# Kernel tuning notes

Measured on AMD Instinct MI355X. Metric: run time of the kernel, lower is better.

Reference implementation:

```python
import jax, jax.numpy as jnp
import numpy as np

VOCAB = 50257
D = 256
BATCH = 8


def setup_inputs() -> dict:
    key = jax.random.key(0)
    k1, k2, k3, k4, k5 = jax.random.split(key, 5)
    initial_ids = jax.random.randint(k1, (BATCH, 1), 0, VOCAB, dtype=jnp.int32)
    state = jax.random.normal(k2, (BATCH, D), dtype=jnp.float32)
    emb = jax.random.normal(k3, (VOCAB, D), dtype=jnp.float32) * 0.02
    W = jax.random.normal(k4, (D, VOCAB), dtype=jnp.float32) * 0.02
    U = jax.random.normal(k5, (D, D), dtype=jnp.float32) * 0.02
    return {"initial_ids": initial_ids, "state": state, "emb": emb,
            "W": W, "U": U, "beam_size": 32, "max_decode_length": 16}


def _logits_fn(ids, state, emb, W, U):
    # Stand-in for the external logits_fn: simple tanh-RNN cell + vocab projection.
    # ids: [b, beam, L], state: [b, beam, d]
    last = ids[:, :, -1]                                       # [b, beam]
    x = jnp.tanh(jnp.einsum('bkd,de->bke', state, U) + emb[last])  # [b, beam, d]
    token_scores = jax.nn.log_softmax(jnp.einsum('bkd,dv->bkv', x, W), axis=-1)
    return token_scores, x


def reference(initial_ids, state, emb, W, U, beam_size, max_decode_length):
    b = initial_ids.shape[0]
    vocab = W.shape[1]
    ids = initial_ids[:, None, :]                # [b, 1, L0]  (beam0 = 1)
    cache = state[:, None, :]                    # [b, 1, d]
    scores = jnp.zeros((b, 1), dtype=jnp.float32)
    for i in range(max_decode_length):           # unrolled, as in the TF original
        beam0 = ids.shape[1]
        token_scores, cache = _logits_fn(ids, cache, emb, W, U)   # [b,beam0,V]
        k = min(beam_size, beam0 * vocab)
        all_scores = (scores[:, :, None] + token_scores).reshape(b, beam0 * vocab)
        top_scores, top_ixs = jax.lax.top_k(all_scores, k)        # sorted, [b,k]
        top_beams = top_ixs // vocab                              # [b,k]
        top_tokens = top_ixs % vocab                              # [b,k]
        ids = jnp.take_along_axis(ids, top_beams[:, :, None], axis=1)
        ids = jnp.concatenate([ids, top_tokens[:, :, None].astype(ids.dtype)], axis=-1)
        cache = jnp.take_along_axis(cache, top_beams[:, :, None], axis=1)
        scores = top_scores
    return ids, scores
```

## Files before the change

kernel.cpp:

```cpp
#include <hip/hip_runtime.h>
#include <math.h>

#define B 8
#define D 256
#define V 50257
#define VP 50304
#define BEAM 32
#define STEPS 16
#define MAXLEN 17
#define FNEG_INF (-3.4e38f)
#define NG 1571
#define NSG 50
#define NSEG 197
#define NLCAP 800
#define SLOTCAP 1600

static_assert((V + 255) / 256 == NSEG, "NSEG mismatch");

struct SchedT {
    int nl, nops, nlev, root, minLeaf;
    int lvlStart[36];
    int leafOff[NLCAP];
    int leafN[NLCAP];
    int sA[NLCAP];
    int sB[NLCAP];
    int sD[NLCAP];
};

constexpr SchedT build_sched() {
    SchedT s{};
    int sOff[64] = {}, sN[64] = {}, sPh[64] = {};
    int vSlot[64] = {}, vLev[64] = {};
    int oA[NLCAP] = {}, oB[NLCAP] = {}, oD[NLCAP] = {}, oL[NLCAP] = {};
    int sp = 0, vp = 0, nl = 0, nops = 0;
    s.minLeaf = 1 << 30;
    sOff[0] = 0; sN[0] = V; sPh[0] = 0; sp = 1;
    while (sp) {
        int i = sp - 1;
        int n = sN[i];
        if (n <= 128) {
            s.leafOff[nl] = sOff[i]; s.leafN[nl] = n;
            if (n < s.minLeaf) s.minLeaf = n;
            vSlot[vp] = nl; vLev[vp] = 0; ++vp; ++nl; --sp; continue;
        }
        int n2 = (n / 2) - ((n / 2) % 8);
        int ph = sPh[i];
        if (ph == 0)      { sPh[i] = 1; sOff[sp] = sOff[i];      sN[sp] = n2;     sPh[sp] = 0; ++sp; }
        else if (ph == 1) { sPh[i] = 2; sOff[sp] = sOff[i] + n2; sN[sp] = n - n2; sPh[sp] = 0; ++sp; }
        else {
            int bI = --vp; int aI = --vp;
            int lev = (vLev[aI] > vLev[bI] ? vLev[aI] : vLev[bI]) + 1;
            oA[nops] = vSlot[aI]; oB[nops] = vSlot[bI]; oD[nops] = NLCAP + nops; oL[nops] = lev;
            vSlot[vp] = NLCAP + nops; vLev[vp] = lev; ++vp; ++nops; --sp;
        }
    }
    s.nl = nl; s.nops = nops; s.root = vSlot[0];
    int maxl = 0;
    for (int k = 0; k < nops; ++k) if (oL[k] > maxl) maxl = oL[k];
    s.nlev = maxl;
    int cnt[36] = {};
    for (int k = 0; k < nops; ++k) cnt[oL[k]]++;
    int run = 0;
    s.lvlStart[0] = 0;
    for (int k = 1; k <= maxl; ++k) { s.lvlStart[k] = run; run += cnt[k]; cnt[k] = s.lvlStart[k]; }
    s.lvlStart[maxl + 1] = run;
    for (int k = 0; k < nops; ++k) { int p = cnt[oL[k]]++; s.sA[p] = oA[k]; s.sB[p] = oB[k]; s.sD[p] = oD[k]; }
    return s;
}

constexpr SchedT SCH = build_sched();
static_assert(SCH.nl <= NLCAP, "leaf overflow");
static_assert(SCH.nops <= NLCAP, "op overflow");
static_assert(SCH.nlev <= 34, "level overflow");
static_assert(SCH.root < SLOTCAP, "slot overflow");
static_assert(SCH.minLeaf >= 8, "leaf < 8 would break 8-lane cluster sum");

__global__ void k_init(const int* __restrict__ initial_ids, const float* __restrict__ state,
                       float* __restrict__ cache, int* __restrict__ ids, float* __restrict__ scores) {
    int b = blockIdx.x, t = threadIdx.x;
    cache[b * D + t] = state[b * D + t];
    if (t == 0) { ids[b * MAXLEN] = initial_ids[b]; scores[b] = 0.f; }
}

__global__ __launch_bounds__(256) void k_embed(const float* __restrict__ cache, const int* __restrict__ ids,
                                               const float* __restrict__ emb, const float* __restrict__ U,
                                               float* __restrict__ x, int step) {
    int rr = blockIdx.x, j = threadIdx.x;
    __shared__ float sc[D];
    sc[j] = cache[rr * D + j];
    __syncthreads();
    int last = ids[rr * MAXLEN + step];
    float acc = 0.f;
    for (int d = 0; d < D; ++d)
        acc = __fadd_rn(acc, __fmul_rn(sc[d], U[d * D + j]));
    float pre = __fadd_rn(acc, emb[(size_t)last * D + j]);
    x[rr * D + j] = (float)tanh((double)pre);
}

__global__ __launch_bounds__(256) void k_trans(const float* __restrict__ x, float* __restrict__ xT) {
    __shared__ float tile[32][33];
    int t = threadIdx.x;
    int tx = t & 31, ty = t >> 5;
    int bx = blockIdx.x * 32, by = blockIdx.y * 32;
#pragma unroll
    for (int i = 0; i < 4; ++i)
        tile[ty + i * 8][tx] = x[(size_t)(by + ty + i * 8) * D + bx + tx];
    __syncthreads();
#pragma unroll
    for (int i = 0; i < 4; ++i)
        xT[(size_t)(bx + ty + i * 8) * 256 + by + tx] = tile[tx][ty + i * 8];
}

__global__ __launch_bounds__(256) void k_gemm(const float* __restrict__ xT, const float* __restrict__ W,
                                              float* __restrict__ L, float* __restrict__ segMax, int rows) {
    int t = threadIdx.x;
    int v = blockIdx.x * 256 + t;
    int r0 = blockIdx.y * 32;
    bool vok = (v < V);
    float acc[32];
#pragma unroll
    for (int r = 0; r < 32; ++r) acc[r] = 0.f;
    for (int d = 0; d < D; ++d) {
        float w = vok ? W[(size_t)d * V + v] : 0.f;
        const float* xp = xT + d * 256 + r0;
#pragma unroll
        for (int r = 0; r < 32; ++r)
            acc[r] = __fadd_rn(acc[r], __fmul_rn(xp[r], w));
    }
#pragma unroll
    for (int r = 0; r < 32; ++r)
        if (vok && r0 + r < rows) L[(size_t)(r0 + r) * VP + v] = acc[r];

    __shared__ float wmax[4][32];
    int wave = t >> 6, lane = t & 63;
#pragma unroll
    for (int r = 0; r < 32; ++r) {
        float mv = vok ? acc[r] : FNEG_INF;
#pragma unroll
        for (int o = 1; o < 64; o <<= 1) mv = fmaxf(mv, __shfl_xor(mv, o));
        if (lane == 0) wmax[wave][r] = mv;
    }
    __syncthreads();
    if (t < 32 && r0 + t < rows) {
        float mv = fmaxf(fmaxf(wmax[0][t], wmax[1][t]), fmaxf(wmax[2][t], wmax[3][t]));
        segMax[(size_t)(r0 + t) * NSEG + blockIdx.x] = mv;
    }
}

__device__ __forceinline__ float Ev(const float* __restrict__ a, float m, int i) {
    return (float)exp((double)__fsub_rn(a[i], m));
}

__global__ __launch_bounds__(1024) void k_post(const float* __restrict__ L, const float* __restrict__ segMax,
                                               const float* __restrict__ scores,
                                               float* __restrict__ candV, int* __restrict__ candI) {
    int rr = blockIdx.x, t = threadIdx.x;
    const float* Lr = L + (size_t)rr * VP;
    __shared__ float mS;
    __shared__ float vals[SLOTCAP];
    __shared__ float gval[NG]; __shared__ int gidx[NG]; __shared__ unsigned gmask[NG];
    __shared__ float gv2[NG]; __shared__ int gi2[NG];
    __shared__ float sgval[64]; __shared__ int sgtok[64]; __shared__ int sggrp[64];

    if (t < 64) {
        float mv = FNEG_INF;
        for (int s = t; s < NSEG; s += 64) mv = fmaxf(mv, segMax[(size_t)rr * NSEG + s]);
#pragma unroll
        for (int o = 1; o < 64; o <<= 1) mv = fmaxf(mv, __shfl_xor(mv, o));
        if (t == 0) mS = mv;
    }
    __syncthreads();
    float m = mS;

    int cl = t >> 3, j = t & 7;
    for (int l = cl; l < SCH.nl; l += 128) {
        int off = SCH.leafOff[l], n = SCH.leafN[l];
        int n8 = n - (n % 8);
        float r = Ev(Lr, m, off + j);
        for (int i = 8; i < n8; i += 8) r = __fadd_rn(r, Ev(Lr, m, off + i + j));
        float s1 = __fadd_rn(r,  __shfl_xor(r, 1));
        float s2 = __fadd_rn(s1, __shfl_xor(s1, 2));
        float s3 = __fadd_rn(s2, __shfl_xor(s2, 4));
        if (j == 0) {
            float res = s3;
            for (int i = n8; i < n; ++i) res = __fadd_rn(res, Ev(Lr, m, off + i));
            vals[l] = res;
        }
    }
    __syncthreads();
    for (int lev = 1; lev <= SCH.nlev; ++lev) {
        for (int i = SCH.lvlStart[lev] + t; i < SCH.lvlStart[lev + 1]; i += 1024)
            vals[SCH.sD[i]] = __fadd_rn(vals[SCH.sA[i]], vals[SCH.sB[i]]);
        __syncthreads();
    }
    float lsf = (float)log((double)vals[SCH.root]);
    float sc = scores[rr];

    int wv = t >> 6, ln = t & 63;
    for (int g2 = wv * 2; g2 < NG; g2 += 32) {
        int g = g2 + (ln >> 5);
        int col = g2 * 32 + ln;
        bool liveg = (g < NG);
        bool live = liveg && (col < V);
        float oval = live ? __fadd_rn(sc, __fsub_rn(__fsub_rn(Lr[col], m), lsf)) : FNEG_INF;
        int oix = live ? col : 0x7fffffff;
        float val = oval; int ix = oix;
#pragma unroll
        for (int o = 1; o < 32; o <<= 1) {
            float v2 = __shfl_xor(val, o);
            int i2 = __shfl_xor(ix, o);
            if (v2 > val || (v2 == val && i2 < ix)) { val = v2; ix = i2; }
        }
        float val2 = (oix == ix) ? FNEG_INF : oval;
        int ix2 = (oix == ix) ? 0x7fffffff : oix;
#pragma unroll
        for (int o = 1; o < 32; o <<= 1) {
            float v2 = __shfl_xor(val2, o);
            int i2 = __shfl_xor(ix2, o);
            if (v2 > val2 || (v2 == val2 && i2 < ix2)) { val2 = v2; ix2 = i2; }
        }
        if (liveg && (ln & 31) == 0) {
            gval[g] = val; gidx[g] = ix; gv2[g] = val2; gi2[g] = ix2; gmask[g] = 0u;
        }
    }
    __syncthreads();

    for (int s2 = wv * 2; s2 < NSG; s2 += 32) {
        int s = s2 + (ln >> 5);
        int g = s2 * 32 + ln;
        bool lives = (s < NSG);
        bool live = lives && (g < NG);
        float val = live ? gval[g] : FNEG_INF;
        int tok = live ? gidx[g] : 0x7fffffff;
        int grp = live ? g : -1;
#pragma unroll
        for (int o = 1; o < 32; o <<= 1) {
            float v2 = __shfl_xor(val, o);
            int t2 = __shfl_xor(tok, o);
            int g3 = __shfl_xor(grp, o);
            if (v2 > val || (v2 == val && t2 < tok)) { val = v2; tok = t2; grp = g3; }
        }
        if (lives && (ln & 31) == 0) { sgval[s] = val; sgtok[s] = tok; sggrp[s] = grp; }
    }
    __syncthreads();
    if (t >= 64) return;

    for (int it = 0; it < 32; ++it) {
        float val = (t < NSG) ? sgval[t] : FNEG_INF;
        int tok = (t < NSG) ? sgtok[t] : 0x7fffffff;
        int grp = (t < NSG) ? sggrp[t] : -1;
#pragma unroll
        for (int o = 1; o < 64; o <<= 1) {
            float v2 = __shfl_xor(val, o);
            int t2 = __shfl_xor(tok, o);
            int g3 = __shfl_xor(grp, o);
            if (v2 > val || (v2 == val && t2 < tok)) { val = v2; tok = t2; grp = g3; }
        }
        int gw = grp, tw = tok;
        unsigned oldmask = gmask[gw];
        unsigned newmask = oldmask | (1u << (tw & 31));
        if (t == 0) {
            candV[rr * 32 + it] = val;
            candI[rr * 32 + it] = tw;
            gmask[gw] = newmask;
        }
        if (__popc(oldmask) == 0) {
            if (t == 0) { gval[gw] = gv2[gw]; gidx[gw] = gi2[gw]; }
        } else {
            int col = gw * 32 + (t & 31);
            bool live = (col < V) && !((newmask >> (t & 31)) & 1u);
            float nv = live ? __fadd_rn(sc, __fsub_rn(__fsub_rn(Lr[col], m), lsf)) : FNEG_INF;
            int nix = live ? col : 0x7fffffff;
#pragma unroll
            for (int o = 1; o < 32; o <<= 1) {
                float v2 = __shfl_xor(nv, o);
                int i2 = __shfl_xor(nix, o);
                if (v2 > nv || (v2 == nv && i2 < nix)) { nv = v2; nix = i2; }
            }
            if (t == 0) { gval[gw] = nv; gidx[gw] = nix; }
        }
        int s = gw >> 5;
        int gg = s * 32 + (t & 31);
        bool lv = (gg < NG);
        float sv = lv ? gval[gg] : FNEG_INF;
        int st = lv ? gidx[gg] : 0x7fffffff;
        int sg2 = lv ? gg : -1;
#pragma unroll
        for (int o = 1; o < 32; o <<= 1) {
            float v2 = __shfl_xor(sv, o);
            int t2 = __shfl_xor(st, o);
            int g3 = __shfl_xor(sg2, o);
            if (v2 > sv || (v2 == sv && t2 < st)) { sv = v2; st = t2; sg2 = g3; }
        }
        if (t == 0) { sgval[s] = sv; sgtok[s] = st; sggrp[s] = sg2; }
    }
}

__global__ __launch_bounds__(256) void k_merge(const float* __restrict__ candV, const int* __restrict__ candI,
                                               float* __restrict__ scoresNxt,
                                               const int* __restrict__ idsCur, int* __restrict__ idsNxt,
                                               const float* __restrict__ x, float* __restrict__ cacheNxt,
                                               int beam0, int step) {
    int b = blockIdx.x, t = threadIdx.x;
    int n = beam0 * BEAM;
    __shared__ float mval[BEAM * BEAM]; __shared__ int mbeam[BEAM * BEAM]; __shared__ int mtok[BEAM * BEAM];
    __shared__ float rv[256]; __shared__ int rk[256]; __shared__ int rs[256];
    __shared__ float wval[BEAM]; __shared__ int wbeam[BEAM]; __shared__ int wtok[BEAM];

    for (int i = t; i < n; i += 256) {
        int beam = i >> 5;
        int rr = b * beam0 + beam;
        mval[i] = candV[rr * BEAM + (i & 31)];
        mbeam[i] = beam;
        mtok[i] = candI[rr * BEAM + (i & 31)];
    }
    __syncthreads();

    for (int it = 0; it < BEAM; ++it) {
        float bv = FNEG_INF; int bk = 0x7fffffff; int bs = -1;
        for (int i = t; i < n; i += 256) {
            float v = mval[i];
            int gi = mbeam[i] * V + mtok[i];
            if (v > bv || (v == bv && gi < bk)) { bv = v; bk = gi; bs = i; }
        }
        rv[t] = bv; rk[t] = bk; rs[t] = bs; __syncthreads();
        for (int o = 128; o > 0; o >>= 1) {
            if (t < o) {
                if (rv[t + o] > rv[t] || (rv[t + o] == rv[t] && rk[t + o] < rk[t])) {
                    rv[t] = rv[t + o]; rk[t] = rk[t + o]; rs[t] = rs[t + o];
                }
            }
            __syncthreads();
        }
        if (t == 0) {
            int w = rs[0];
            wval[it] = rv[0]; wbeam[it] = mbeam[w]; wtok[it] = mtok[w];
            mval[w] = FNEG_INF;
        }
        __syncthreads();
    }

    if (t < BEAM) {
        scoresNxt[b * BEAM + t] = wval[t];
        int src = b * beam0 + wbeam[t];
        for (int u = 0; u <= step; ++u)
            idsNxt[(b * BEAM + t) * MAXLEN + u] = idsCur[src * MAXLEN + u];
        idsNxt[(b * BEAM + t) * MAXLEN + step + 1] = wtok[t];
    }
    __syncthreads();
    for (int j = 0; j < BEAM; ++j) {
        int src = b * beam0 + wbeam[j];
        cacheNxt[(size_t)(b * BEAM + j) * D + t] = x[(size_t)src * D + t];
    }
}

__global__ void k_out(const int* __restrict__ ids, const float* __restrict__ scores, float* __restrict__ out) {
    int t = blockIdx.x * 256 + threadIdx.x;
    const int NI = B * BEAM * MAXLEN;
    if (t < NI) out[t] = (float)ids[t];
    else if (t < NI + B * BEAM) out[t] = scores[t - NI];
}

extern "C" void kernel_launch(void* const* d_in, const int* in_sizes, int n_in,
                              void* d_out, int out_size, void* d_ws, size_t ws_size,
                              hipStream_t stream) {
    const int* initial_ids = (const int*)d_in[0];
    const float* state = (const float*)d_in[1];
    const float* emb = (const float*)d_in[2];
    const float* W = (const float*)d_in[3];
    const float* U = (const float*)d_in[4];

    char* ws = (char*)d_ws;
    size_t off = 0;
    float* L = (float*)(ws + off);       off += (size_t)256 * VP * 4;
    float* x = (float*)(ws + off);       off += 256 * D * 4;
    float* xT = (float*)(ws + off);      off += 256 * D * 4;
    float* cacheA = (float*)(ws + off);  off += 256 * D * 4;
    float* cacheB = (float*)(ws + off);  off += 256 * D * 4;
    float* scoresA = (float*)(ws + off); off += 256 * 4;
    float* scoresB = (float*)(ws + off); off += 256 * 4;
    int* idsA = (int*)(ws + off);        off += 256 * MAXLEN * 4;
    int* idsB = (int*)(ws + off);        off += 256 * MAXLEN * 4;
    float* candV = (float*)(ws + off);   off += 256 * 32 * 4;
    int* candI = (int*)(ws + off);       off += 256 * 32 * 4;
    float* segMax = (float*)(ws + off);  off += (size_t)256 * NSEG * 4;

    if (ws_size < off) return;

    k_init<<<B, 256, 0, stream>>>(initial_ids, state, cacheA, idsA, scoresA);

    float* cCur = cacheA; float* cNxt = cacheB;
    float* sCur = scoresA; float* sNxt = scoresB;
    int* iCur = idsA; int* iNxt = idsB;

    for (int step = 0; step < STEPS; ++step) {
        int beam0 = (step == 0) ? 1 : BEAM;
        int rows = B * beam0;

        k_embed<<<rows, 256, 0, stream>>>(cCur, iCur, emb, U, x, step);

        dim3 gt(8, 8);
        k_trans<<<gt, 256, 0, stream>>>(x, xT);

        dim3 g(NSEG, (rows + 31) / 32);
        k_gemm<<<g, 256, 0, stream>>>(xT, W, L, segMax, rows);

        k_post<<<rows, 1024, 0, stream>>>(L, segMax, sCur, candV, candI);
        k_merge<<<B, 256, 0, stream>>>(candV, candI, sNxt, iCur, iNxt, x, cNxt, beam0, step);

        float* tf; int* ti;
        tf = cCur; cCur = cNxt; cNxt = tf;
        tf = sCur; sCur = sNxt; sNxt = tf;
        ti = iCur; iCur = iNxt; iNxt = ti;
    }

    k_out<<<(B * BEAM * MAXLEN + B * BEAM + 255) / 256, 256, 0, stream>>>(iCur, sCur, (float*)d_out);
}
```

Measured before the change: 4.882 ms.

## Split post-processing into two-half logsumexp kernel and LDS-staged top-k kernel

The single per-row post kernel becomes two kernels. k_lsf builds its summation schedule for each half of the vocabulary and runs both halves as separate blocks, giving twice as many blocks for the double-precision exp reduction. The split point equals the original tree's root split, so the summation order stays the same. k_top then stages the logits in chunks through a 64KB shared buffer and computes each group's top-2 with a per-thread scan instead of wave shuffles. The cost is an extra launch, the logits being read twice, and heavy shared-memory use that limits occupancy.

```diff
diff --git a/kernel.cpp b/kernel.cpp
--- a/kernel.cpp
+++ b/kernel.cpp
@@ -14,6 +14,8 @@
 #define NSEG 197
 #define NLCAP 800
 #define SLOTCAP 1600
+#define NSPLIT 25128
+#define CHUNK 16384
 
 static_assert((V + 255) / 256 == NSEG, "NSEG mismatch");
 
@@ -27,14 +29,14 @@
     int sD[NLCAP];
 };
 
-constexpr SchedT build_sched() {
+constexpr SchedT build_sched(int off0, int n0) {
     SchedT s{};
     int sOff[64] = {}, sN[64] = {}, sPh[64] = {};
     int vSlot[64] = {}, vLev[64] = {};
     int oA[NLCAP] = {}, oB[NLCAP] = {}, oD[NLCAP] = {}, oL[NLCAP] = {};
     int sp = 0, vp = 0, nl = 0, nops = 0;
     s.minLeaf = 1 << 30;
-    sOff[0] = 0; sN[0] = V; sPh[0] = 0; sp = 1;
+    sOff[0] = off0; sN[0] = n0; sPh[0] = 0; sp = 1;
     while (sp) {
         int i = sp - 1;
         int n = sN[i];
@@ -68,12 +70,12 @@
     return s;
 }
 
-constexpr SchedT SCH = build_sched();
-static_assert(SCH.nl <= NLCAP, "leaf overflow");
-static_assert(SCH.nops <= NLCAP, "op overflow");
-static_assert(SCH.nlev <= 34, "level overflow");
-static_assert(SCH.root < SLOTCAP, "slot overflow");
-static_assert(SCH.minLeaf >= 8, "leaf < 8 would break 8-lane cluster sum");
+constexpr SchedT SCHL = build_sched(0, NSPLIT);
+constexpr SchedT SCHR = build_sched(NSPLIT, V - NSPLIT);
+static_assert(SCHL.nl <= NLCAP && SCHR.nl <= NLCAP, "leaf overflow");
+static_assert(SCHL.nops <= NLCAP && SCHR.nops <= NLCAP, "op overflow");
+static_assert(SCHL.nlev <= 34 && SCHR.nlev <= 34, "level overflow");
+static_assert(SCHL.minLeaf >= 8 && SCHR.minLeaf >= 8, "leaf < 8 breaks 8-lane cluster");
 
 __global__ void k_init(const int* __restrict__ initial_ids, const float* __restrict__ state,
                        float* __restrict__ cache, int* __restrict__ ids, float* __restrict__ scores) {
@@ -151,16 +153,12 @@
     return (float)exp((double)__fsub_rn(a[i], m));
 }
 
-__global__ __launch_bounds__(1024) void k_post(const float* __restrict__ L, const float* __restrict__ segMax,
-                                               const float* __restrict__ scores,
-                                               float* __restrict__ candV, int* __restrict__ candI) {
-    int rr = blockIdx.x, t = threadIdx.x;
+__global__ __launch_bounds__(1024) void k_lsf(const float* __restrict__ L, const float* __restrict__ segMax,
+                                              float* __restrict__ pSum) {
+    int rr = blockIdx.x, half = blockIdx.y, t = threadIdx.x;
     const float* Lr = L + (size_t)rr * VP;
     __shared__ float mS;
     __shared__ float vals[SLOTCAP];
-    __shared__ float gval[NG]; __shared__ int gidx[NG]; __shared__ unsigned gmask[NG];
-    __shared__ float gv2[NG]; __shared__ int gi2[NG];
-    __shared__ float sgval[64]; __shared__ int sgtok[64]; __shared__ int sggrp[64];
 
     if (t < 64) {
         float mv = FNEG_INF;
@@ -172,9 +170,19 @@
     __syncthreads();
     float m = mS;
 
+    const int* leafOff = half ? SCHR.leafOff : SCHL.leafOff;
+    const int* leafN   = half ? SCHR.leafN   : SCHL.leafN;
+    const int* sA      = half ? SCHR.sA      : SCHL.sA;
+    const int* sB      = half ? SCHR.sB      : SCHL.sB;
+    const int* sD      = half ? SCHR.sD      : SCHL.sD;
+    const int* lvlStart= half ? SCHR.lvlStart: SCHL.lvlStart;
+    int nl   = half ? SCHR.nl   : SCHL.nl;
+    int nlev = half ? SCHR.nlev : SCHL.nlev;
+    int root = half ? SCHR.root : SCHL.root;
+
     int cl = t >> 3, j = t & 7;
-    for (int l = cl; l < SCH.nl; l += 128) {
-        int off = SCH.leafOff[l], n = SCH.leafN[l];
+    for (int l = cl; l < nl; l += 128) {
+        int off = leafOff[l], n = leafN[l];
         int n8 = n - (n % 8);
         float r = Ev(Lr, m, off + j);
         for (int i = 8; i < n8; i += 8) r = __fadd_rn(r, Ev(Lr, m, off + i + j));
@@ -188,43 +196,67 @@
         }
     }
     __syncthreads();
-    for (int lev = 1; lev <= SCH.nlev; ++lev) {
-        for (int i = SCH.lvlStart[lev] + t; i < SCH.lvlStart[lev + 1]; i += 1024)
-            vals[SCH.sD[i]] = __fadd_rn(vals[SCH.sA[i]], vals[SCH.sB[i]]);
+    for (int lev = 1; lev <= nlev; ++lev) {
+        for (int i = lvlStart[lev] + t; i < lvlStart[lev + 1]; i += 1024)
+            vals[sD[i]] = __fadd_rn(vals[sA[i]], vals[sB[i]]);
         __syncthreads();
     }
-    float lsf = (float)log((double)vals[SCH.root]);
+    if (t == 0) pSum[rr * 2 + half] = vals[root];
+}
+
+__global__ __launch_bounds__(1024) void k_top(const float* __restrict__ L, const float* __restrict__ segMax,
+                                              const float* __restrict__ pSum, const float* __restrict__ scores,
+                                              float* __restrict__ candV, int* __restrict__ candI) {
+    int rr = blockIdx.x, t = threadIdx.x;
+    const float* Lr = L + (size_t)rr * VP;
+    __shared__ float mS;
+    __shared__ float buf[CHUNK];
+    __shared__ float gval[NG]; __shared__ int gidx[NG]; __shared__ unsigned gmask[NG];
+    __shared__ float gv2[NG]; __shared__ int gi2[NG];
+    __shared__ float sgval[64]; __shared__ int sgtok[64]; __shared__ int sggrp[64];
+
+    if (t < 64) {
+        float mv = FNEG_INF;
+        for (int s = t; s < NSEG; s += 64) mv = fmaxf(mv, segMax[(size_t)rr * NSEG + s]);
+#pragma unroll
+        for (int o = 1; o < 64; o <<= 1) mv = fmaxf(mv, __shfl_xor(mv, o));
+        if (t == 0) mS = mv;
+    }
+    __syncthreads();
+    float m = mS;
+    float lsf = (float)log((double)__fadd_rn(pSum[rr * 2 + 0], pSum[rr * 2 + 1]));
     float sc = scores[rr];
 
+    for (int c = 0; c < (V + CHUNK - 1) / CHUNK; ++c) {
+        int base = c * CHUNK;
+        int cnt = V - base; if (cnt > CHUNK) cnt = CHUNK;
+        int cnt4 = (cnt + 3) >> 2;
+        const float4* L4 = (const float4*)(Lr + base);
+        float4* B4 = (float4*)buf;
+        for (int i = t; i < cnt4; i += 1024) B4[i] = L4[i];
+        __syncthreads();
+        int gBase = base >> 5;
+        int gCnt = (cnt + 31) >> 5;
+        for (int g = gBase + t; g < gBase + gCnt; g += 1024) {
+            int local = (g - gBase) * 32;
+            float b1v = FNEG_INF, b2v = FNEG_INF; int b1i = 0x7fffffff, b2i = 0x7fffffff;
+            for (int k = 0; k < 32; ++k) {
+                int kk = (k + t) & 31;
+                int col = g * 32 + kk;
+                if (col >= V) continue;
+                float val = __fadd_rn(sc, __fsub_rn(__fsub_rn(buf[local + kk], m), lsf));
+                if (val > b1v || (val == b1v && col < b1i)) {
+                    b2v = b1v; b2i = b1i; b1v = val; b1i = col;
+                } else if (val > b2v || (val == b2v && col < b2i)) {
+                    b2v = val; b2i = col;
+                }
+            }
+            gval[g] = b1v; gidx[g] = b1i; gv2[g] = b2v; gi2[g] = b2i; gmask[g] = 0u;
+        }
+        __syncthreads();
+    }
+
     int wv = t >> 6, ln = t & 63;
-    for (int g2 = wv * 2; g2 < NG; g2 += 32) {
-        int g = g2 + (ln >> 5);
-        int col = g2 * 32 + ln;
-        bool liveg = (g < NG);
-        bool live = liveg && (col < V);
-        float oval = live ? __fadd_rn(sc, __fsub_rn(__fsub_rn(Lr[col], m), lsf)) : FNEG_INF;
-        int oix = live ? col : 0x7fffffff;
-        float val = oval; int ix = oix;
-#pragma unroll
-        for (int o = 1; o < 32; o <<= 1) {
-            float v2 = __shfl_xor(val, o);
-            int i2 = __shfl_xor(ix, o);
-            if (v2 > val || (v2 == val && i2 < ix)) { val = v2; ix = i2; }
-        }
-        float val2 = (oix == ix) ? FNEG_INF : oval;
-        int ix2 = (oix == ix) ? 0x7fffffff : oix;
-#pragma unroll
-        for (int o = 1; o < 32; o <<= 1) {
-            float v2 = __shfl_xor(val2, o);
-            int i2 = __shfl_xor(ix2, o);
-            if (v2 > val2 || (v2 == val2 && i2 < ix2)) { val2 = v2; ix2 = i2; }
-        }
-        if (liveg && (ln & 31) == 0) {
-            gval[g] = val; gidx[g] = ix; gv2[g] = val2; gi2[g] = ix2; gmask[g] = 0u;
-        }
-    }
-    __syncthreads();
-
     for (int s2 = wv * 2; s2 < NSG; s2 += 32) {
         int s = s2 + (ln >> 5);
         int g = s2 * 32 + ln;
@@ -384,6 +416,7 @@
     float* candV = (float*)(ws + off);   off += 256 * 32 * 4;
     int* candI = (int*)(ws + off);       off += 256 * 32 * 4;
     float* segMax = (float*)(ws + off);  off += (size_t)256 * NSEG * 4;
+    float* pSum = (float*)(ws + off);    off += 256 * 2 * 4;
 
     if (ws_size < off) return;
 
@@ -405,7 +438,9 @@
         dim3 g(NSEG, (rows + 31) / 32);
         k_gemm<<<g, 256, 0, stream>>>(xT, W, L, segMax, rows);
 
-        k_post<<<rows, 1024, 0, stream>>>(L, segMax, sCur, candV, candI);
+        dim3 gl(rows, 2);
+        k_lsf<<<gl, 1024, 0, stream>>>(L, segMax, pSum);
+        k_top<<<rows, 1024, 0, stream>>>(L, segMax, pSum, sCur, candV, candI);
         k_merge<<<B, 256, 0, stream>>>(candV, candI, sNxt, iCur, iNxt, x, cNxt, beam0, step);
 
         float* tf; int* ti;
```

Result: faster. 4.187 ms (-14.2%).
